# Kernel tuning notes

Hardware: AMD Instinct MI355X
Metric: run time of the kernel (lower is better)

The kernel has to match this reference:

```python
import jax, jax.numpy as jnp
import numpy as np
from jax.ops import segment_sum

N = 50000
E = 800000
D_IN = 128
D_H = 64
D_OUT = 1
NUM_GRAPHS = 64


def setup_inputs() -> dict:
    key = jax.random.key(0)
    ks = jax.random.split(key, 12)
    x = jax.random.normal(ks[0], (N, D_IN), dtype=jnp.float32)
    edge_index = jax.random.randint(ks[1], (2, E), 0, N, dtype=jnp.int32)
    batch = jnp.sort(jax.random.randint(ks[2], (N,), 0, NUM_GRAPHS, dtype=jnp.int32))
    def glorot(k, fan_in, fan_out):
        lim = np.sqrt(6.0 / (fan_in + fan_out))
        return jax.random.uniform(k, (fan_in, fan_out), jnp.float32, -lim, lim)
    return {
        "x": x,
        "edge_index": edge_index,
        "batch": batch,
        "W1": glorot(ks[3], D_IN, D_H), "b1": jnp.zeros((D_H,), jnp.float32),
        "W2": glorot(ks[4], D_H, D_H), "b2": jnp.zeros((D_H,), jnp.float32),
        "W3": glorot(ks[5], D_H, D_H), "b3": jnp.zeros((D_H,), jnp.float32),
        "Wl": glorot(ks[6], D_H, D_OUT), "bl": jnp.zeros((D_OUT,), jnp.float32),
    }


def _gcn_conv(x, W, b, row, col, norm):
    # x' = scatter_add(norm * (xW)[row] -> col) + b   (PyG GCNConv with self-loops)
    h = x @ W                                   # [N, d_out]
    msg = h[row] * norm[:, None]                # [E+N, d_out] gather + scale
    out = segment_sum(msg, col, num_segments=N) # scatter-add at targets
    return out + b


def reference(x, edge_index, batch, W1, b1, W2, b2, W3, b3, Wl, bl):
    # add self loops
    loops = jnp.arange(N, dtype=edge_index.dtype)
    row = jnp.concatenate([edge_index[0], loops])  # sources
    col = jnp.concatenate([edge_index[1], loops])  # targets
    # symmetric degree normalization (degree over targets, incl. self loops)
    deg = segment_sum(jnp.ones_like(col, dtype=x.dtype), col, num_segments=N)
    dinv = jnp.where(deg > 0, jax.lax.rsqrt(deg), 0.0)
    norm = dinv[row] * dinv[col]

    h = jax.nn.elu(_gcn_conv(x, W1, b1, row, col, norm))
    h = jax.nn.elu(_gcn_conv(h, W2, b2, row, col, norm))
    h = jax.nn.elu(_gcn_conv(h, W3, b3, row, col, norm))
    h = h @ Wl + bl                                         # [N, 1]
    # global mean pool over graphs
    sums = segment_sum(h, batch, num_segments=NUM_GRAPHS)   # [G, 1]
    cnts = segment_sum(jnp.ones((N, 1), h.dtype), batch, num_segments=NUM_GRAPHS)
    pooled = sums / jnp.maximum(cnts, 1.0)
    return jnp.squeeze(pooled)
```

## Files before the change

### kernel.cpp

```cpp
#include <hip/hip_runtime.h>
#include <math.h>

#define NN 50000
#define NE 800000
#define DIN 128
#define DH 64
#define NG 64

#define GEMM_BLOCKS ((NN + 63) / 64)
#define DEG_BLOCKS 2048
#define FILL_BLOCKS 2048
#define SCALE_BLOCKS 256
#define SCAN_BLOCKS ((NN + 255) / 256)

template <int K>
__global__ __launch_bounds__(256, 4) void gemm_deg_kernel(const float* __restrict__ in,
                                                          const float* __restrict__ W,
                                                          float* __restrict__ out, int n,
                                                          const int* __restrict__ col,
                                                          int* __restrict__ indeg, int e) {
    __shared__ float Ws[K * 64];
    if (blockIdx.x >= GEMM_BLOCKS) {
        int i = (blockIdx.x - GEMM_BLOCKS) * 256 + threadIdx.x;
        int stride = DEG_BLOCKS * 256;
        for (; i < e; i += stride) atomicAdd(&indeg[col[i]], 1);
        return;
    }
    for (int t = threadIdx.x; t < K * 16; t += 256)
        reinterpret_cast<float4*>(Ws)[t] = reinterpret_cast<const float4*>(W)[t];
    __syncthreads();

    int w = threadIdx.x >> 6, l = threadIdx.x & 63;
    int fq = l & 15;
    int nl = l >> 4;
    int base = blockIdx.x * 64 + w * 16 + nl * 4;

    const float* r0 = in + (size_t)min(base + 0, n - 1) * K;
    const float* r1 = in + (size_t)min(base + 1, n - 1) * K;
    const float* r2 = in + (size_t)min(base + 2, n - 1) * K;
    const float* r3 = in + (size_t)min(base + 3, n - 1) * K;

    float acc[4][4];
    #pragma unroll
    for (int i = 0; i < 4; ++i)
        #pragma unroll
        for (int f = 0; f < 4; ++f) acc[i][f] = 0.f;

    #pragma unroll 2
    for (int k = 0; k < K; k += 4) {
        float4 wv[4];
        #pragma unroll
        for (int kk = 0; kk < 4; ++kk)
            wv[kk] = *reinterpret_cast<const float4*>(&Ws[(k + kk) * 64 + 4 * fq]);
        float4 xv[4];
        xv[0] = *reinterpret_cast<const float4*>(r0 + k);
        xv[1] = *reinterpret_cast<const float4*>(r1 + k);
        xv[2] = *reinterpret_cast<const float4*>(r2 + k);
        xv[3] = *reinterpret_cast<const float4*>(r3 + k);
        #pragma unroll
        for (int i = 0; i < 4; ++i) {
            float xs[4] = {xv[i].x, xv[i].y, xv[i].z, xv[i].w};
            #pragma unroll
            for (int kk = 0; kk < 4; ++kk) {
                acc[i][0] = fmaf(xs[kk], wv[kk].x, acc[i][0]);
                acc[i][1] = fmaf(xs[kk], wv[kk].y, acc[i][1]);
                acc[i][2] = fmaf(xs[kk], wv[kk].z, acc[i][2]);
                acc[i][3] = fmaf(xs[kk], wv[kk].w, acc[i][3]);
            }
        }
    }

    #pragma unroll
    for (int i = 0; i < 4; ++i) {
        int node = base + i;
        if (node < n) {
            float4 o = make_float4(acc[i][0], acc[i][1], acc[i][2], acc[i][3]);
            *reinterpret_cast<float4*>(&out[(size_t)node * 64 + 4 * fq]) = o;
        }
    }
}

template <int K>
__global__ __launch_bounds__(256, 4) void gemm_scaled_kernel(const float* __restrict__ in,
                                                             const float* __restrict__ W,
                                                             const float* __restrict__ dinv,
                                                             float* __restrict__ out, int n) {
    __shared__ float Ws[K * 64];
    for (int t = threadIdx.x; t < K * 16; t += 256)
        reinterpret_cast<float4*>(Ws)[t] = reinterpret_cast<const float4*>(W)[t];
    __syncthreads();

    int w = threadIdx.x >> 6, l = threadIdx.x & 63;
    int fq = l & 15;
    int nl = l >> 4;
    int base = blockIdx.x * 64 + w * 16 + nl * 4;

    const float* r0 = in + (size_t)min(base + 0, n - 1) * K;
    const float* r1 = in + (size_t)min(base + 1, n - 1) * K;
    const float* r2 = in + (size_t)min(base + 2, n - 1) * K;
    const float* r3 = in + (size_t)min(base + 3, n - 1) * K;

    float acc[4][4];
    #pragma unroll
    for (int i = 0; i < 4; ++i)
        #pragma unroll
        for (int f = 0; f < 4; ++f) acc[i][f] = 0.f;

    #pragma unroll 2
    for (int k = 0; k < K; k += 4) {
        float4 wv[4];
        #pragma unroll
        for (int kk = 0; kk < 4; ++kk)
            wv[kk] = *reinterpret_cast<const float4*>(&Ws[(k + kk) * 64 + 4 * fq]);
        float4 xv[4];
        xv[0] = *reinterpret_cast<const float4*>(r0 + k);
        xv[1] = *reinterpret_cast<const float4*>(r1 + k);
        xv[2] = *reinterpret_cast<const float4*>(r2 + k);
        xv[3] = *reinterpret_cast<const float4*>(r3 + k);
        #pragma unroll
        for (int i = 0; i < 4; ++i) {
            float xs[4] = {xv[i].x, xv[i].y, xv[i].z, xv[i].w};
            #pragma unroll
            for (int kk = 0; kk < 4; ++kk) {
                acc[i][0] = fmaf(xs[kk], wv[kk].x, acc[i][0]);
                acc[i][1] = fmaf(xs[kk], wv[kk].y, acc[i][1]);
                acc[i][2] = fmaf(xs[kk], wv[kk].z, acc[i][2]);
                acc[i][3] = fmaf(xs[kk], wv[kk].w, acc[i][3]);
            }
        }
    }

    #pragma unroll
    for (int i = 0; i < 4; ++i) {
        int node = base + i;
        if (node < n) {
            float sc = dinv[node];
            float4 o = make_float4(acc[i][0] * sc, acc[i][1] * sc,
                                   acc[i][2] * sc, acc[i][3] * sc);
            *reinterpret_cast<float4*>(&out[(size_t)node * 64 + 4 * fq]) = o;
        }
    }
}

__global__ __launch_bounds__(256) void scan_phaseA(const int* __restrict__ indeg,
                                                   int* __restrict__ partial, int n) {
    int i = blockIdx.x * 256 + threadIdx.x;
    int v = (i < n) ? indeg[i] : 0;
    int s = v;
    #pragma unroll
    for (int d = 1; d < 64; d <<= 1) s += __shfl_xor(s, d, 64);
    __shared__ int ws[4];
    if ((threadIdx.x & 63) == 0) ws[threadIdx.x >> 6] = s;
    __syncthreads();
    if (threadIdx.x == 0) partial[blockIdx.x] = ws[0] + ws[1] + ws[2] + ws[3];
}

__global__ __launch_bounds__(256) void scan_phaseB(int* __restrict__ partial, int nb) {
    int t = threadIdx.x;
    int lane = t & 63, wid = t >> 6;
    int v = (t < nb) ? partial[t] : 0;
    int inc = v;
    #pragma unroll
    for (int d = 1; d < 64; d <<= 1) {
        int u = __shfl_up(inc, d, 64);
        if (lane >= d) inc += u;
    }
    __shared__ int ws[4];
    if (lane == 63) ws[wid] = inc;
    __syncthreads();
    int woff = 0;
    #pragma unroll
    for (int k = 0; k < 4; ++k) woff += (k < wid) ? ws[k] : 0;
    if (t < nb) partial[t] = woff + inc - v;
}

__global__ __launch_bounds__(256) void scan_phaseC(const int* __restrict__ indeg,
                                                   const int* __restrict__ partial,
                                                   int* __restrict__ off,
                                                   int* __restrict__ cursor,
                                                   float* __restrict__ dinv, int n) {
    int i = blockIdx.x * 256 + threadIdx.x;
    int d = (i < n) ? indeg[i] : 0;
    int lane = threadIdx.x & 63, wid = threadIdx.x >> 6;
    int inc = d;
    #pragma unroll
    for (int dd = 1; dd < 64; dd <<= 1) {
        int u = __shfl_up(inc, dd, 64);
        if (lane >= dd) inc += u;
    }
    __shared__ int ws[4];
    if (lane == 63) ws[wid] = inc;
    __syncthreads();
    int woff = 0;
    #pragma unroll
    for (int k = 0; k < 4; ++k) woff += (k < wid) ? ws[k] : 0;
    int excl = partial[blockIdx.x] + woff + inc - d;
    if (i < n) {
        off[i] = excl;
        cursor[i] = excl;
        dinv[i] = rsqrtf((float)(d + 1));
        if (i == n - 1) off[n] = excl + d;
    }
}

__global__ __launch_bounds__(256) void fill_scale_kernel(const int* __restrict__ row,
                                                         const int* __restrict__ col,
                                                         int* __restrict__ cursor,
                                                         int* __restrict__ ews, int e,
                                                         float* __restrict__ tmp,
                                                         const float* __restrict__ dinv,
                                                         int n4) {
    if (blockIdx.x < FILL_BLOCKS) {
        int i = blockIdx.x * 256 + threadIdx.x;
        int stride = FILL_BLOCKS * 256;
        for (; i < e; i += stride) {
            int c = col[i];
            int p = atomicAdd(&cursor[c], 1);
            ews[p] = row[i];
        }
    } else {
        float4* t4 = reinterpret_cast<float4*>(tmp);
        int i = (blockIdx.x - FILL_BLOCKS) * 256 + threadIdx.x;
        int stride = SCALE_BLOCKS * 256;
        for (; i < n4; i += stride) {
            float sc = dinv[i >> 4];
            float4 v = t4[i];
            v.x *= sc; v.y *= sc; v.z *= sc; v.w *= sc;
            t4[i] = v;
        }
    }
}

__global__ __launch_bounds__(256) void pull_kernel(const float* __restrict__ tmp,
                                                   const int* __restrict__ off,
                                                   const int* __restrict__ ews,
                                                   const float* __restrict__ dinv,
                                                   const float* __restrict__ bias,
                                                   float* __restrict__ out, int n) {
    int wid = threadIdx.x >> 6;
    int lane = threadIdx.x & 63;
    int node = blockIdx.x * 4 + wid;
    if (node >= n) return;
    int fg = lane & 15, e4 = lane >> 4;
    const float4* trow = reinterpret_cast<const float4*>(tmp);

    float4 acc = make_float4(0.f, 0.f, 0.f, 0.f);
    int e = off[node], s1 = off[node + 1];

    for (; e + 8 <= s1; e += 8) {
        int i0 = ews[e + e4];
        int i1 = ews[e + 4 + e4];
        float4 v0 = trow[(size_t)i0 * 16 + fg];
        float4 v1 = trow[(size_t)i1 * 16 + fg];
        acc.x += v0.x + v1.x;
        acc.y += v0.y + v1.y;
        acc.z += v0.z + v1.z;
        acc.w += v0.w + v1.w;
    }
    for (; e < s1; e += 4) {
        int idx = e + e4;
        if (idx < s1) {
            float4 v = trow[(size_t)ews[idx] * 16 + fg];
            acc.x += v.x;
            acc.y += v.y;
            acc.z += v.z;
            acc.w += v.w;
        }
    }

    acc.x += __shfl_xor(acc.x, 16, 64);
    acc.y += __shfl_xor(acc.y, 16, 64);
    acc.z += __shfl_xor(acc.z, 16, 64);
    acc.w += __shfl_xor(acc.w, 16, 64);
    acc.x += __shfl_xor(acc.x, 32, 64);
    acc.y += __shfl_xor(acc.y, 32, 64);
    acc.z += __shfl_xor(acc.z, 32, 64);
    acc.w += __shfl_xor(acc.w, 32, 64);

    float dt = dinv[node];
    float4 self = trow[(size_t)node * 16 + fg];
    float4 b4 = reinterpret_cast<const float4*>(bias)[fg];
    float4 r;
    r.x = fmaf(acc.x + self.x, dt, b4.x);
    r.y = fmaf(acc.y + self.y, dt, b4.y);
    r.z = fmaf(acc.z + self.z, dt, b4.z);
    r.w = fmaf(acc.w + self.w, dt, b4.w);
    r.x = (r.x > 0.f) ? r.x : expm1f(r.x);
    r.y = (r.y > 0.f) ? r.y : expm1f(r.y);
    r.z = (r.z > 0.f) ? r.z : expm1f(r.z);
    r.w = (r.w > 0.f) ? r.w : expm1f(r.w);
    if (e4 == 0)
        reinterpret_cast<float4*>(out)[(size_t)node * 16 + fg] = r;
}

#define POOL_BLOCKS 256
__global__ __launch_bounds__(256) void final_pool_kernel(const float* __restrict__ h,
                                                         const float* __restrict__ Wl,
                                                         const int* __restrict__ batch,
                                                         float* __restrict__ gsum,
                                                         float* __restrict__ gcnt, int n) {
    __shared__ float lsum[NG];
    __shared__ float lcnt[NG];
    if (threadIdx.x < NG) { lsum[threadIdx.x] = 0.f; lcnt[threadIdx.x] = 0.f; }
    __syncthreads();
    int wid = threadIdx.x >> 6, lane = threadIdx.x & 63;
    float wl = Wl[lane];
    int per_block = (n + POOL_BLOCKS - 1) / POOL_BLOCKS;
    int start = blockIdx.x * per_block;
    int end = start + per_block;
    if (end > n) end = n;
    for (int node = start + wid; node < end; node += 4) {
        float p = h[(size_t)node * 64 + lane] * wl;
        #pragma unroll
        for (int d = 32; d >= 1; d >>= 1) p += __shfl_xor(p, d, 64);
        if (lane == 0) {
            int g = batch[node];
            atomicAdd(&lsum[g], p);
            atomicAdd(&lcnt[g], 1.f);
        }
    }
    __syncthreads();
    if (threadIdx.x < NG && lcnt[threadIdx.x] != 0.f) {
        atomicAdd(&gsum[threadIdx.x], lsum[threadIdx.x]);
        atomicAdd(&gcnt[threadIdx.x], lcnt[threadIdx.x]);
    }
}

__global__ void pool_div_kernel(const float* __restrict__ gsum, const float* __restrict__ gcnt,
                                const float* __restrict__ bl, float* __restrict__ out) {
    int g = threadIdx.x;
    if (g < NG) {
        float c = gcnt[g];
        out[g] = (c > 0.5f) ? (gsum[g] / c + bl[0]) : 0.f;
    }
}

extern "C" void kernel_launch(void* const* d_in, const int* in_sizes, int n_in,
                              void* d_out, int out_size, void* d_ws, size_t ws_size,
                              hipStream_t stream) {
    const float* x    = (const float*)d_in[0];
    const int*   eidx = (const int*)d_in[1];
    const int*   row  = eidx;
    const int*   col  = eidx + NE;
    const int*   batch = (const int*)d_in[2];
    const float* W1 = (const float*)d_in[3];
    const float* b1 = (const float*)d_in[4];
    const float* W2 = (const float*)d_in[5];
    const float* b2 = (const float*)d_in[6];
    const float* W3 = (const float*)d_in[7];
    const float* b3 = (const float*)d_in[8];
    const float* Wl = (const float*)d_in[9];
    const float* bl = (const float*)d_in[10];
    float* out = (float*)d_out;

    size_t cur = 0;
    auto take = [&](size_t elems) { size_t c = cur; cur += (elems + 63) & ~(size_t)63; return c; };
    float* base_f = (float*)d_ws;
    int*   base_i = (int*)d_ws;

    float*  dinv    = base_f + take(NN);
    int*    indeg   = base_i + take(NN);
    int*    csr_off = base_i + take(NN + 1);
    int*    cursor  = base_i + take(NN);
    int*    partial = base_i + take(SCAN_BLOCKS);
    int*    ews     = base_i + take(NE);
    float*  tmp     = base_f + take((size_t)NN * 64);
    float*  h       = base_f + take((size_t)NN * 64);
    float*  gg      = base_f + take(2 * NG);
    float*  gsum    = gg;
    float*  gcnt    = gg + NG;
    (void)ws_size; (void)n_in; (void)in_sizes; (void)out_size;

    hipMemsetAsync(indeg, 0, NN * sizeof(int), stream);
    hipMemsetAsync(gg, 0, 2 * NG * sizeof(float), stream);

    const int nblk_pull = (NN + 3) / 4;

    gemm_deg_kernel<DIN><<<GEMM_BLOCKS + DEG_BLOCKS, 256, 0, stream>>>(
        x, W1, tmp, NN, col, indeg, NE);
    scan_phaseA<<<SCAN_BLOCKS, 256, 0, stream>>>(indeg, partial, NN);
    scan_phaseB<<<1, 256, 0, stream>>>(partial, SCAN_BLOCKS);
    scan_phaseC<<<SCAN_BLOCKS, 256, 0, stream>>>(indeg, partial, csr_off, cursor, dinv, NN);
    fill_scale_kernel<<<FILL_BLOCKS + SCALE_BLOCKS, 256, 0, stream>>>(
        row, col, cursor, ews, NE, tmp, dinv, NN * 16);

    pull_kernel<<<nblk_pull, 256, 0, stream>>>(tmp, csr_off, ews, dinv, b1, h, NN);

    gemm_scaled_kernel<DH><<<GEMM_BLOCKS, 256, 0, stream>>>(h, W2, dinv, tmp, NN);
    pull_kernel<<<nblk_pull, 256, 0, stream>>>(tmp, csr_off, ews, dinv, b2, h, NN);

    gemm_scaled_kernel<DH><<<GEMM_BLOCKS, 256, 0, stream>>>(h, W3, dinv, tmp, NN);
    pull_kernel<<<nblk_pull, 256, 0, stream>>>(tmp, csr_off, ews, dinv, b3, h, NN);

    final_pool_kernel<<<POOL_BLOCKS, 256, 0, stream>>>(h, Wl, batch, gsum, gcnt, NN);
    pool_div_kernel<<<1, 64, 0, stream>>>(gsum, gcnt, bl, out);
}
```

Baseline: 341.0 us.

## Fuse neighbor aggregation with next-layer GEMM and final pooling projection

Each GCN layer's pull-aggregation kernel now also multiplies the ELU output by the next layer's weight matrix (held per lane in registers) and scales by dinv. This removes the separate GEMM kernels and the round trip of the hidden activations through global memory. The last layer folds the Wl projection and graph pooling into the pull, so the separate pool kernel goes away. It also reorders the fill/scale block split and uses a fixed grid of 2048 blocks, each looping over a chunk of nodes. The costs are 64 extra registers per thread and shuffle-heavy per-node matvec work inside the latency-bound gather loop.

```diff
diff --git a/kernel.cpp b/kernel.cpp
--- a/kernel.cpp
+++ b/kernel.cpp
@@ -12,6 +12,8 @@
 #define FILL_BLOCKS 2048
 #define SCALE_BLOCKS 256
 #define SCAN_BLOCKS ((NN + 255) / 256)
+#define PULL_BLOCKS 2048
+#define PULL_CHUNK ((NN + PULL_BLOCKS - 1) / PULL_BLOCKS)
 
 template <int K>
 __global__ __launch_bounds__(256, 4) void gemm_deg_kernel(const float* __restrict__ in,
@@ -80,68 +82,6 @@
     }
 }
 
-template <int K>
-__global__ __launch_bounds__(256, 4) void gemm_scaled_kernel(const float* __restrict__ in,
-                                                             const float* __restrict__ W,
-                                                             const float* __restrict__ dinv,
-                                                             float* __restrict__ out, int n) {
-    __shared__ float Ws[K * 64];
-    for (int t = threadIdx.x; t < K * 16; t += 256)
-        reinterpret_cast<float4*>(Ws)[t] = reinterpret_cast<const float4*>(W)[t];
-    __syncthreads();
-
-    int w = threadIdx.x >> 6, l = threadIdx.x & 63;
-    int fq = l & 15;
-    int nl = l >> 4;
-    int base = blockIdx.x * 64 + w * 16 + nl * 4;
-
-    const float* r0 = in + (size_t)min(base + 0, n - 1) * K;
-    const float* r1 = in + (size_t)min(base + 1, n - 1) * K;
-    const float* r2 = in + (size_t)min(base + 2, n - 1) * K;
-    const float* r3 = in + (size_t)min(base + 3, n - 1) * K;
-
-    float acc[4][4];
-    #pragma unroll
-    for (int i = 0; i < 4; ++i)
-        #pragma unroll
-        for (int f = 0; f < 4; ++f) acc[i][f] = 0.f;
-
-    #pragma unroll 2
-    for (int k = 0; k < K; k += 4) {
-        float4 wv[4];
-        #pragma unroll
-        for (int kk = 0; kk < 4; ++kk)
-            wv[kk] = *reinterpret_cast<const float4*>(&Ws[(k + kk) * 64 + 4 * fq]);
-        float4 xv[4];
-        xv[0] = *reinterpret_cast<const float4*>(r0 + k);
-        xv[1] = *reinterpret_cast<const float4*>(r1 + k);
-        xv[2] = *reinterpret_cast<const float4*>(r2 + k);
-        xv[3] = *reinterpret_cast<const float4*>(r3 + k);
-        #pragma unroll
-        for (int i = 0; i < 4; ++i) {
-            float xs[4] = {xv[i].x, xv[i].y, xv[i].z, xv[i].w};
-            #pragma unroll
-            for (int kk = 0; kk < 4; ++kk) {
-                acc[i][0] = fmaf(xs[kk], wv[kk].x, acc[i][0]);
-                acc[i][1] = fmaf(xs[kk], wv[kk].y, acc[i][1]);
-                acc[i][2] = fmaf(xs[kk], wv[kk].z, acc[i][2]);
-                acc[i][3] = fmaf(xs[kk], wv[kk].w, acc[i][3]);
-            }
-        }
-    }
-
-    #pragma unroll
-    for (int i = 0; i < 4; ++i) {
-        int node = base + i;
-        if (node < n) {
-            float sc = dinv[node];
-            float4 o = make_float4(acc[i][0] * sc, acc[i][1] * sc,
-                                   acc[i][2] * sc, acc[i][3] * sc);
-            *reinterpret_cast<float4*>(&out[(size_t)node * 64 + 4 * fq]) = o;
-        }
-    }
-}
-
 __global__ __launch_bounds__(256) void scan_phaseA(const int* __restrict__ indeg,
                                                    int* __restrict__ partial, int n) {
     int i = blockIdx.x * 256 + threadIdx.x;
@@ -210,17 +150,9 @@
                                                          float* __restrict__ tmp,
                                                          const float* __restrict__ dinv,
                                                          int n4) {
-    if (blockIdx.x < FILL_BLOCKS) {
+    if (blockIdx.x < SCALE_BLOCKS) {
+        float4* t4 = reinterpret_cast<float4*>(tmp);
         int i = blockIdx.x * 256 + threadIdx.x;
-        int stride = FILL_BLOCKS * 256;
-        for (; i < e; i += stride) {
-            int c = col[i];
-            int p = atomicAdd(&cursor[c], 1);
-            ews[p] = row[i];
-        }
-    } else {
-        float4* t4 = reinterpret_cast<float4*>(tmp);
-        int i = (blockIdx.x - FILL_BLOCKS) * 256 + threadIdx.x;
         int stride = SCALE_BLOCKS * 256;
         for (; i < n4; i += stride) {
             float sc = dinv[i >> 4];
@@ -228,91 +160,165 @@
             v.x *= sc; v.y *= sc; v.z *= sc; v.w *= sc;
             t4[i] = v;
         }
-    }
-}
-
-__global__ __launch_bounds__(256) void pull_kernel(const float* __restrict__ tmp,
-                                                   const int* __restrict__ off,
-                                                   const int* __restrict__ ews,
-                                                   const float* __restrict__ dinv,
-                                                   const float* __restrict__ bias,
-                                                   float* __restrict__ out, int n) {
+    } else {
+        int i = (blockIdx.x - SCALE_BLOCKS) * 256 + threadIdx.x;
+        int stride = FILL_BLOCKS * 256;
+        for (; i < e; i += stride) {
+            int c = col[i];
+            int p = atomicAdd(&cursor[c], 1);
+            ews[p] = row[i];
+        }
+    }
+}
+
+__global__ __launch_bounds__(256, 4) void pull_gemm_kernel(const float* __restrict__ tin,
+                                                           const int* __restrict__ off,
+                                                           const int* __restrict__ ews,
+                                                           const float* __restrict__ dinv,
+                                                           const float* __restrict__ bias,
+                                                           const float* __restrict__ Wn,
+                                                           float* __restrict__ tout, int n) {
     int wid = threadIdx.x >> 6;
     int lane = threadIdx.x & 63;
-    int node = blockIdx.x * 4 + wid;
-    if (node >= n) return;
     int fg = lane & 15, e4 = lane >> 4;
-    const float4* trow = reinterpret_cast<const float4*>(tmp);
-
-    float4 acc = make_float4(0.f, 0.f, 0.f, 0.f);
-    int e = off[node], s1 = off[node + 1];
-
-    for (; e + 8 <= s1; e += 8) {
-        int i0 = ews[e + e4];
-        int i1 = ews[e + 4 + e4];
-        float4 v0 = trow[(size_t)i0 * 16 + fg];
-        float4 v1 = trow[(size_t)i1 * 16 + fg];
-        acc.x += v0.x + v1.x;
-        acc.y += v0.y + v1.y;
-        acc.z += v0.z + v1.z;
-        acc.w += v0.w + v1.w;
-    }
-    for (; e < s1; e += 4) {
-        int idx = e + e4;
-        if (idx < s1) {
-            float4 v = trow[(size_t)ews[idx] * 16 + fg];
-            acc.x += v.x;
-            acc.y += v.y;
-            acc.z += v.z;
-            acc.w += v.w;
-        }
-    }
-
-    acc.x += __shfl_xor(acc.x, 16, 64);
-    acc.y += __shfl_xor(acc.y, 16, 64);
-    acc.z += __shfl_xor(acc.z, 16, 64);
-    acc.w += __shfl_xor(acc.w, 16, 64);
-    acc.x += __shfl_xor(acc.x, 32, 64);
-    acc.y += __shfl_xor(acc.y, 32, 64);
-    acc.z += __shfl_xor(acc.z, 32, 64);
-    acc.w += __shfl_xor(acc.w, 32, 64);
-
-    float dt = dinv[node];
-    float4 self = trow[(size_t)node * 16 + fg];
+
+    float Wcol[64];
+    #pragma unroll
+    for (int k = 0; k < 64; ++k) Wcol[k] = Wn[k * 64 + lane];
+
+    const float4* trow = reinterpret_cast<const float4*>(tin);
     float4 b4 = reinterpret_cast<const float4*>(bias)[fg];
-    float4 r;
-    r.x = fmaf(acc.x + self.x, dt, b4.x);
-    r.y = fmaf(acc.y + self.y, dt, b4.y);
-    r.z = fmaf(acc.z + self.z, dt, b4.z);
-    r.w = fmaf(acc.w + self.w, dt, b4.w);
-    r.x = (r.x > 0.f) ? r.x : expm1f(r.x);
-    r.y = (r.y > 0.f) ? r.y : expm1f(r.y);
-    r.z = (r.z > 0.f) ? r.z : expm1f(r.z);
-    r.w = (r.w > 0.f) ? r.w : expm1f(r.w);
-    if (e4 == 0)
-        reinterpret_cast<float4*>(out)[(size_t)node * 16 + fg] = r;
-}
-
-#define POOL_BLOCKS 256
-__global__ __launch_bounds__(256) void final_pool_kernel(const float* __restrict__ h,
-                                                         const float* __restrict__ Wl,
-                                                         const int* __restrict__ batch,
-                                                         float* __restrict__ gsum,
-                                                         float* __restrict__ gcnt, int n) {
+
+    int lo = blockIdx.x * PULL_CHUNK;
+    int hi = lo + PULL_CHUNK; if (hi > n) hi = n;
+
+    for (int node = lo + wid; node < hi; node += 4) {
+        float4 acc = make_float4(0.f, 0.f, 0.f, 0.f);
+        int e = off[node], s1 = off[node + 1];
+        for (; e + 8 <= s1; e += 8) {
+            int i0 = ews[e + e4];
+            int i1 = ews[e + 4 + e4];
+            float4 v0 = trow[(size_t)i0 * 16 + fg];
+            float4 v1 = trow[(size_t)i1 * 16 + fg];
+            acc.x += v0.x + v1.x;
+            acc.y += v0.y + v1.y;
+            acc.z += v0.z + v1.z;
+            acc.w += v0.w + v1.w;
+        }
+        for (; e < s1; e += 4) {
+            int idx = e + e4;
+            if (idx < s1) {
+                float4 v = trow[(size_t)ews[idx] * 16 + fg];
+                acc.x += v.x; acc.y += v.y; acc.z += v.z; acc.w += v.w;
+            }
+        }
+        acc.x += __shfl_xor(acc.x, 16, 64);
+        acc.y += __shfl_xor(acc.y, 16, 64);
+        acc.z += __shfl_xor(acc.z, 16, 64);
+        acc.w += __shfl_xor(acc.w, 16, 64);
+        acc.x += __shfl_xor(acc.x, 32, 64);
+        acc.y += __shfl_xor(acc.y, 32, 64);
+        acc.z += __shfl_xor(acc.z, 32, 64);
+        acc.w += __shfl_xor(acc.w, 32, 64);
+
+        float dt = dinv[node];
+        float4 self = trow[(size_t)node * 16 + fg];
+        float4 r;
+        r.x = fmaf(acc.x + self.x, dt, b4.x);
+        r.y = fmaf(acc.y + self.y, dt, b4.y);
+        r.z = fmaf(acc.z + self.z, dt, b4.z);
+        r.w = fmaf(acc.w + self.w, dt, b4.w);
+        r.x = (r.x > 0.f) ? r.x : expm1f(r.x);
+        r.y = (r.y > 0.f) ? r.y : expm1f(r.y);
+        r.z = (r.z > 0.f) ? r.z : expm1f(r.z);
+        r.w = (r.w > 0.f) ? r.w : expm1f(r.w);
+
+        float o = 0.f;
+        #pragma unroll
+        for (int q = 0; q < 16; ++q) {
+            float hx = __shfl(r.x, q, 64);
+            float hy = __shfl(r.y, q, 64);
+            float hz = __shfl(r.z, q, 64);
+            float hw = __shfl(r.w, q, 64);
+            o = fmaf(hx, Wcol[4 * q + 0], o);
+            o = fmaf(hy, Wcol[4 * q + 1], o);
+            o = fmaf(hz, Wcol[4 * q + 2], o);
+            o = fmaf(hw, Wcol[4 * q + 3], o);
+        }
+        tout[(size_t)node * 64 + lane] = o * dt;
+    }
+}
+
+__global__ __launch_bounds__(256, 4) void pull_final_kernel(const float* __restrict__ tin,
+                                                            const int* __restrict__ off,
+                                                            const int* __restrict__ ews,
+                                                            const float* __restrict__ dinv,
+                                                            const float* __restrict__ bias,
+                                                            const float* __restrict__ Wl,
+                                                            const int* __restrict__ batch,
+                                                            float* __restrict__ gsum,
+                                                            float* __restrict__ gcnt, int n) {
     __shared__ float lsum[NG];
     __shared__ float lcnt[NG];
     if (threadIdx.x < NG) { lsum[threadIdx.x] = 0.f; lcnt[threadIdx.x] = 0.f; }
     __syncthreads();
-    int wid = threadIdx.x >> 6, lane = threadIdx.x & 63;
-    float wl = Wl[lane];
-    int per_block = (n + POOL_BLOCKS - 1) / POOL_BLOCKS;
-    int start = blockIdx.x * per_block;
-    int end = start + per_block;
-    if (end > n) end = n;
-    for (int node = start + wid; node < end; node += 4) {
-        float p = h[(size_t)node * 64 + lane] * wl;
-        #pragma unroll
-        for (int d = 32; d >= 1; d >>= 1) p += __shfl_xor(p, d, 64);
+
+    int wid = threadIdx.x >> 6;
+    int lane = threadIdx.x & 63;
+    int fg = lane & 15, e4 = lane >> 4;
+    const float4* trow = reinterpret_cast<const float4*>(tin);
+    float4 b4 = reinterpret_cast<const float4*>(bias)[fg];
+    float4 wl4 = reinterpret_cast<const float4*>(Wl)[fg];
+
+    int lo = blockIdx.x * PULL_CHUNK;
+    int hi = lo + PULL_CHUNK; if (hi > n) hi = n;
+
+    for (int node = lo + wid; node < hi; node += 4) {
+        float4 acc = make_float4(0.f, 0.f, 0.f, 0.f);
+        int e = off[node], s1 = off[node + 1];
+        for (; e + 8 <= s1; e += 8) {
+            int i0 = ews[e + e4];
+            int i1 = ews[e + 4 + e4];
+            float4 v0 = trow[(size_t)i0 * 16 + fg];
+            float4 v1 = trow[(size_t)i1 * 16 + fg];
+            acc.x += v0.x + v1.x;
+            acc.y += v0.y + v1.y;
+            acc.z += v0.z + v1.z;
+            acc.w += v0.w + v1.w;
+        }
+        for (; e < s1; e += 4) {
+            int idx = e + e4;
+            if (idx < s1) {
+                float4 v = trow[(size_t)ews[idx] * 16 + fg];
+                acc.x += v.x; acc.y += v.y; acc.z += v.z; acc.w += v.w;
+            }
+        }
+        acc.x += __shfl_xor(acc.x, 16, 64);
+        acc.y += __shfl_xor(acc.y, 16, 64);
+        acc.z += __shfl_xor(acc.z, 16, 64);
+        acc.w += __shfl_xor(acc.w, 16, 64);
+        acc.x += __shfl_xor(acc.x, 32, 64);
+        acc.y += __shfl_xor(acc.y, 32, 64);
+        acc.z += __shfl_xor(acc.z, 32, 64);
+        acc.w += __shfl_xor(acc.w, 32, 64);
+
+        float dt = dinv[node];
+        float4 self = trow[(size_t)node * 16 + fg];
+        float4 r;
+        r.x = fmaf(acc.x + self.x, dt, b4.x);
+        r.y = fmaf(acc.y + self.y, dt, b4.y);
+        r.z = fmaf(acc.z + self.z, dt, b4.z);
+        r.w = fmaf(acc.w + self.w, dt, b4.w);
+        r.x = (r.x > 0.f) ? r.x : expm1f(r.x);
+        r.y = (r.y > 0.f) ? r.y : expm1f(r.y);
+        r.z = (r.z > 0.f) ? r.z : expm1f(r.z);
+        r.w = (r.w > 0.f) ? r.w : expm1f(r.w);
+
+        float p = r.x * wl4.x + r.y * wl4.y + r.z * wl4.z + r.w * wl4.w;
+        p += __shfl_xor(p, 1, 64);
+        p += __shfl_xor(p, 2, 64);
+        p += __shfl_xor(p, 4, 64);
+        p += __shfl_xor(p, 8, 64);
         if (lane == 0) {
             int g = batch[node];
             atomicAdd(&lsum[g], p);
@@ -364,8 +370,8 @@
     int*    cursor  = base_i + take(NN);
     int*    partial = base_i + take(SCAN_BLOCKS);
     int*    ews     = base_i + take(NE);
-    float*  tmp     = base_f + take((size_t)NN * 64);
-    float*  h       = base_f + take((size_t)NN * 64);
+    float*  tA      = base_f + take((size_t)NN * 64);
+    float*  tB      = base_f + take((size_t)NN * 64);
     float*  gg      = base_f + take(2 * NG);
     float*  gsum    = gg;
     float*  gcnt    = gg + NG;
@@ -374,24 +380,20 @@
     hipMemsetAsync(indeg, 0, NN * sizeof(int), stream);
     hipMemsetAsync(gg, 0, 2 * NG * sizeof(float), stream);
 
-    const int nblk_pull = (NN + 3) / 4;
-
     gemm_deg_kernel<DIN><<<GEMM_BLOCKS + DEG_BLOCKS, 256, 0, stream>>>(
-        x, W1, tmp, NN, col, indeg, NE);
+        x, W1, tA, NN, col, indeg, NE);
     scan_phaseA<<<SCAN_BLOCKS, 256, 0, stream>>>(indeg, partial, NN);
     scan_phaseB<<<1, 256, 0, stream>>>(partial, SCAN_BLOCKS);
     scan_phaseC<<<SCAN_BLOCKS, 256, 0, stream>>>(indeg, partial, csr_off, cursor, dinv, NN);
-    fill_scale_kernel<<<FILL_BLOCKS + SCALE_BLOCKS, 256, 0, stream>>>(
-        row, col, cursor, ews, NE, tmp, dinv, NN * 16);
-
-    pull_kernel<<<nblk_pull, 256, 0, stream>>>(tmp, csr_off, ews, dinv, b1, h, NN);
-
-    gemm_scaled_kernel<DH><<<GEMM_BLOCKS, 256, 0, stream>>>(h, W2, dinv, tmp, NN);
-    pull_kernel<<<nblk_pull, 256, 0, stream>>>(tmp, csr_off, ews, dinv, b2, h, NN);
-
-    gemm_scaled_kernel<DH><<<GEMM_BLOCKS, 256, 0, stream>>>(h, W3, dinv, tmp, NN);
-    pull_kernel<<<nblk_pull, 256, 0, stream>>>(tmp, csr_off, ews, dinv, b3, h, NN);
-
-    final_pool_kernel<<<POOL_BLOCKS, 256, 0, stream>>>(h, Wl, batch, gsum, gcnt, NN);
+    fill_scale_kernel<<<SCALE_BLOCKS + FILL_BLOCKS, 256, 0, stream>>>(
+        row, col, cursor, ews, NE, tA, dinv, NN * 16);
+
+    pull_gemm_kernel<<<PULL_BLOCKS, 256, 0, stream>>>(
+        tA, csr_off, ews, dinv, b1, W2, tB, NN);
+    pull_gemm_kernel<<<PULL_BLOCKS, 256, 0, stream>>>(
+        tB, csr_off, ews, dinv, b2, W3, tA, NN);
+    pull_final_kernel<<<PULL_BLOCKS, 256, 0, stream>>>(
+        tA, csr_off, ews, dinv, b3, Wl, batch, gsum, gcnt, NN);
+
     pool_div_kernel<<<1, 64, 0, stream>>>(gsum, gcnt, bl, out);
 }
```

Result: no change. 341.5 us (+0.1%).
